# Kernel tuning notes

Hardware: AMD Instinct MI355X
Metric: run time of the kernel (lower is better)

Reference implementation:

```python
import jax, jax.numpy as jnp
import numpy as np


def setup_inputs() -> dict:
    key = jax.random.key(0)
    k1, k2 = jax.random.split(key)
    mesh_3D = jax.random.uniform(k1, (100, 100, 100, 3), dtype=jnp.float32)
    receiver_pos = jax.random.uniform(k2, (128, 3), dtype=jnp.float32)
    return {"mesh_3D": mesh_3D, "receiver_pos": receiver_pos}


def reference(mesh_3D, receiver_pos):
    # Flatten mesh to [L, 3]
    pts = mesh_3D.reshape(-1, 3)
    L = pts.shape[0]
    B = receiver_pos.shape[0]
    # Squared distances [B, L]; argmin of sqrt(d2) == argmin of d2 (sqrt is monotone),
    # so skipping the sqrt gives the same indices as the torch code.
    d2 = jnp.sum((receiver_pos[:, None, :] - pts[None, :, :]) ** 2, axis=-1)
    min_index = jnp.argmin(d2, axis=1).astype(jnp.int32)  # [B]
    # One-hot over the mesh. The original loop scatters with the *whole* min_index
    # tensor (zero-initialized) at every iteration, so for B > 1 index 0 also ends
    # up set to 1. We reproduce that behavior faithfully.
    one_hot = jnp.zeros((L, 1), dtype=pts.dtype).at[min_index, 0].set(1.0)
    if B > 1:
        one_hot = one_hot.at[0, 0].set(1.0)
    closest_points = pts[min_index]  # [B, 3]
    input_tensor = jnp.concatenate([pts, one_hot], axis=1).astype(jnp.float32)  # [L, 4]
    return input_tensor, closest_points, min_index
```

## Files before the change

### kernel.cpp

```cpp
#include <hip/hip_runtime.h>
#include <hip/hip_bf16.h>


#define NRECV 128
#define TILE 512
#define BLK 256
#define NGRP 4

typedef unsigned long long u64;

__global__ __launch_bounds__(BLK) void k_argmin_fill(
    const float* __restrict__ pts, const float* __restrict__ recv,
    u64* __restrict__ stage, float* __restrict__ out, int L, int ntiles) {
  __shared__ float4 sp4[TILE];
  __shared__ u64 sm[NGRP][NRECV];

  const int tid = threadIdx.x;
  const int g = tid >> 6;
  const int c = tid & 63;

  const float rx0 = recv[c * 3 + 0];
  const float ry0 = recv[c * 3 + 1];
  const float rz0 = recv[c * 3 + 2];
  const float rx1 = recv[(c + 64) * 3 + 0];
  const float ry1 = recv[(c + 64) * 3 + 1];
  const float rz1 = recv[(c + 64) * 3 + 2];

  float b0 = 3.4e38f, b1 = 3.4e38f;
  int i0 = 0, i1 = 0;

  for (int t = blockIdx.x; t < ntiles; t += gridDim.x) {
    const int base = t * TILE;
    const int cnt = min(TILE, L - base);

    for (int q = tid; q < cnt; q += BLK) {
      const int gi = base + q;
      float4 v;
      v.x = pts[3 * gi + 0];
      v.y = pts[3 * gi + 1];
      v.z = pts[3 * gi + 2];
      v.w = 0.0f;
      sp4[q] = v;
      reinterpret_cast<float4*>(out)[gi] = v;
    }
    __syncthreads();

#pragma unroll 4
    for (int p = g; p < cnt; p += NGRP) {
      const float4 q = sp4[p];
      const float dx0 = q.x - rx0, dy0 = q.y - ry0, dz0 = q.z - rz0;
      const float d0 = fmaf(dz0, dz0, fmaf(dy0, dy0, dx0 * dx0));
      const float dx1 = q.x - rx1, dy1 = q.y - ry1, dz1 = q.z - rz1;
      const float d1 = fmaf(dz1, dz1, fmaf(dy1, dy1, dx1 * dx1));
      const bool c0 = d0 < b0;
      b0 = c0 ? d0 : b0;
      i0 = c0 ? (base + p) : i0;
      const bool c1 = d1 < b1;
      b1 = c1 ? d1 : b1;
      i1 = c1 ? (base + p) : i1;
    }
    __syncthreads();
  }

  sm[g][c] = ((u64)__float_as_uint(b0) << 32) | (unsigned int)i0;
  sm[g][c + 64] = ((u64)__float_as_uint(b1) << 32) | (unsigned int)i1;
  __syncthreads();
  if (tid < NRECV) {
    u64 best = sm[0][tid];
#pragma unroll
    for (int k = 1; k < NGRP; ++k) {
      u64 o = sm[k][tid];
      best = o < best ? o : best;
    }
    stage[(size_t)blockIdx.x * NRECV + tid] = best;
  }
}

__global__ __launch_bounds__(BLK) void k_finalize(
    const u64* __restrict__ stage, int nblocks,
    const float* __restrict__ pts, float* __restrict__ out, int L) {
  const int r = blockIdx.x;
  const int tid = threadIdx.x;

  u64 best = ~0ull;
  for (int j = tid; j < nblocks; j += BLK) {
    u64 k = stage[(size_t)j * NRECV + r];
    best = k < best ? k : best;
  }
  for (int off = 32; off > 0; off >>= 1) {
    u64 o = __shfl_down(best, off);
    best = o < best ? o : best;
  }
  __shared__ u64 w[BLK / 64];
  if ((tid & 63) == 0) w[tid >> 6] = best;
  __syncthreads();
  if (tid == 0) {
#pragma unroll
    for (int i = 1; i < BLK / 64; ++i) {
      u64 o = w[i];
      best = o < best ? o : best;
    }
    const unsigned int idx = (unsigned int)(best & 0xffffffffu);
    const size_t Lo = (size_t)L * 4;
    out[Lo + (size_t)r * 3 + 0] = pts[(size_t)idx * 3 + 0];
    out[Lo + (size_t)r * 3 + 1] = pts[(size_t)idx * 3 + 1];
    out[Lo + (size_t)r * 3 + 2] = pts[(size_t)idx * 3 + 2];
    out[Lo + (size_t)NRECV * 3 + r] = (float)idx;
    out[(size_t)idx * 4 + 3] = 1.0f;
    if (r == 0) out[3] = 1.0f;
  }
}

extern "C" void kernel_launch(void* const* d_in, const int* in_sizes, int n_in,
                              void* d_out, int out_size, void* d_ws, size_t ws_size,
                              hipStream_t stream) {
  const float* pts = (const float*)d_in[0];
  const float* recv = (const float*)d_in[1];
  float* out = (float*)d_out;

  const int L = in_sizes[0] / 3;
  const int ntiles = (L + TILE - 1) / TILE;

  int nb1 = 1024;
  if ((size_t)nb1 * NRECV * sizeof(u64) > ws_size) {
    nb1 = (int)(ws_size / (NRECV * sizeof(u64)));
    if (nb1 < 1) nb1 = 1;
  }
  if (nb1 > ntiles) nb1 = ntiles;

  u64* stage = (u64*)d_ws;

  k_argmin_fill<<<nb1, BLK, 0, stream>>>(pts, recv, stage, out, L, ntiles);
  k_finalize<<<NRECV, BLK, 0, stream>>>(stage, nb1, pts, out, L);
}
```

Before: 96.82 us.

## Use 4 receivers per thread and atomicMin banks for cross-block argmin

The main kernel now uses 512-thread blocks. Each thread handles 4 receivers (32-lane halves of each wave take alternating points), and the two half-wave results are merged with a shuffle. Instead of writing per-block partials to a large staging buffer scanned by a 128-block finalize, blocks atomicMin packed (distance,index) keys into 4 padded banks of cells. A tiny single-block finalize then reads those cells, at the cost of an extra init kernel launch and atomic contention. A sentinel point is also written past the end of a partial tile so the paired-lane loop does not read garbage.

```diff
diff --git a/kernel.cpp b/kernel.cpp
--- a/kernel.cpp
+++ b/kernel.cpp
@@ -1,114 +1,119 @@
 #include <hip/hip_runtime.h>
-#include <hip/hip_bf16.h>
 
 
 #define NRECV 128
 #define TILE 512
-#define BLK 256
-#define NGRP 4
+#define BLK 512
+#define NWAVE (BLK / 64)
+#define CELL_STRIDE 16
 
 typedef unsigned long long u64;
 
-__global__ __launch_bounds__(BLK) void k_argmin_fill(
+__global__ __launch_bounds__(128) void k_init(u64* __restrict__ cells, int n) {
+  int i = blockIdx.x * 128 + threadIdx.x;
+  if (i < n) cells[i] = ~0ull;
+}
+
+__global__ __launch_bounds__(BLK) void k_main(
     const float* __restrict__ pts, const float* __restrict__ recv,
-    u64* __restrict__ stage, float* __restrict__ out, int L, int ntiles) {
-  __shared__ float4 sp4[TILE];
-  __shared__ u64 sm[NGRP][NRECV];
+    u64* __restrict__ cells, int nbanks, float* __restrict__ out,
+    int L, int ntiles) {
+  __shared__ float4 sp4[TILE + 1];
+  __shared__ u64 sm[NWAVE][NRECV];
 
   const int tid = threadIdx.x;
   const int g = tid >> 6;
-  const int c = tid & 63;
+  const int c = tid & 31;
+  const int ph = (tid >> 5) & 1;
 
-  const float rx0 = recv[c * 3 + 0];
-  const float ry0 = recv[c * 3 + 1];
-  const float rz0 = recv[c * 3 + 2];
-  const float rx1 = recv[(c + 64) * 3 + 0];
-  const float ry1 = recv[(c + 64) * 3 + 1];
-  const float rz1 = recv[(c + 64) * 3 + 2];
+  float rx[4], ry[4], rz[4];
+#pragma unroll
+  for (int k = 0; k < 4; ++k) {
+    rx[k] = recv[(c + 32 * k) * 3 + 0];
+    ry[k] = recv[(c + 32 * k) * 3 + 1];
+    rz[k] = recv[(c + 32 * k) * 3 + 2];
+  }
 
-  float b0 = 3.4e38f, b1 = 3.4e38f;
-  int i0 = 0, i1 = 0;
+  float bd[4] = {1e30f, 1e30f, 1e30f, 1e30f};
+  int bi[4] = {0, 0, 0, 0};
 
   for (int t = blockIdx.x; t < ntiles; t += gridDim.x) {
     const int base = t * TILE;
     const int cnt = min(TILE, L - base);
 
-    for (int q = tid; q < cnt; q += BLK) {
-      const int gi = base + q;
+    if (tid < cnt) {
+      const int gi = base + tid;
       float4 v;
       v.x = pts[3 * gi + 0];
       v.y = pts[3 * gi + 1];
       v.z = pts[3 * gi + 2];
       v.w = 0.0f;
-      sp4[q] = v;
+      sp4[tid] = v;
       reinterpret_cast<float4*>(out)[gi] = v;
     }
+    if (tid == 0 && cnt < TILE)
+      sp4[cnt] = make_float4(1e30f, 1e30f, 1e30f, 0.0f);
     __syncthreads();
 
-#pragma unroll 4
-    for (int p = g; p < cnt; p += NGRP) {
+#pragma unroll 2
+    for (int p2 = 2 * g; p2 < cnt; p2 += 2 * NWAVE) {
+      const int p = p2 + ph;
       const float4 q = sp4[p];
-      const float dx0 = q.x - rx0, dy0 = q.y - ry0, dz0 = q.z - rz0;
-      const float d0 = fmaf(dz0, dz0, fmaf(dy0, dy0, dx0 * dx0));
-      const float dx1 = q.x - rx1, dy1 = q.y - ry1, dz1 = q.z - rz1;
-      const float d1 = fmaf(dz1, dz1, fmaf(dy1, dy1, dx1 * dx1));
-      const bool c0 = d0 < b0;
-      b0 = c0 ? d0 : b0;
-      i0 = c0 ? (base + p) : i0;
-      const bool c1 = d1 < b1;
-      b1 = c1 ? d1 : b1;
-      i1 = c1 ? (base + p) : i1;
+#pragma unroll
+      for (int k = 0; k < 4; ++k) {
+        const float dx = q.x - rx[k];
+        const float dy = q.y - ry[k];
+        const float dz = q.z - rz[k];
+        const float d = fmaf(dz, dz, fmaf(dy, dy, dx * dx));
+        const bool cc = d < bd[k];
+        bd[k] = cc ? d : bd[k];
+        bi[k] = cc ? (base + p) : bi[k];
+      }
     }
     __syncthreads();
   }
 
-  sm[g][c] = ((u64)__float_as_uint(b0) << 32) | (unsigned int)i0;
-  sm[g][c + 64] = ((u64)__float_as_uint(b1) << 32) | (unsigned int)i1;
+  u64 key[4];
+#pragma unroll
+  for (int k = 0; k < 4; ++k) {
+    key[k] = ((u64)__float_as_uint(bd[k]) << 32) | (unsigned int)bi[k];
+    const u64 o = __shfl_xor(key[k], 32, 64);
+    key[k] = o < key[k] ? o : key[k];
+  }
+  if (ph == 0) {
+#pragma unroll
+    for (int k = 0; k < 4; ++k) sm[g][c + 32 * k] = key[k];
+  }
   __syncthreads();
   if (tid < NRECV) {
     u64 best = sm[0][tid];
 #pragma unroll
-    for (int k = 1; k < NGRP; ++k) {
-      u64 o = sm[k][tid];
+    for (int w = 1; w < NWAVE; ++w) {
+      const u64 o = sm[w][tid];
       best = o < best ? o : best;
     }
-    stage[(size_t)blockIdx.x * NRECV + tid] = best;
+    const int bank = blockIdx.x & (nbanks - 1);
+    atomicMin(&cells[(size_t)(bank * NRECV + tid) * CELL_STRIDE], best);
   }
 }
 
-__global__ __launch_bounds__(BLK) void k_finalize(
-    const u64* __restrict__ stage, int nblocks,
+__global__ __launch_bounds__(128) void k_finalize(
+    const u64* __restrict__ cells, int nbanks,
     const float* __restrict__ pts, float* __restrict__ out, int L) {
-  const int r = blockIdx.x;
-  const int tid = threadIdx.x;
-
+  const int r = threadIdx.x;
   u64 best = ~0ull;
-  for (int j = tid; j < nblocks; j += BLK) {
-    u64 k = stage[(size_t)j * NRECV + r];
-    best = k < best ? k : best;
-  }
-  for (int off = 32; off > 0; off >>= 1) {
-    u64 o = __shfl_down(best, off);
+  for (int b = 0; b < nbanks; ++b) {
+    const u64 o = cells[(size_t)(b * NRECV + r) * CELL_STRIDE];
     best = o < best ? o : best;
   }
-  __shared__ u64 w[BLK / 64];
-  if ((tid & 63) == 0) w[tid >> 6] = best;
-  __syncthreads();
-  if (tid == 0) {
-#pragma unroll
-    for (int i = 1; i < BLK / 64; ++i) {
-      u64 o = w[i];
-      best = o < best ? o : best;
-    }
-    const unsigned int idx = (unsigned int)(best & 0xffffffffu);
-    const size_t Lo = (size_t)L * 4;
-    out[Lo + (size_t)r * 3 + 0] = pts[(size_t)idx * 3 + 0];
-    out[Lo + (size_t)r * 3 + 1] = pts[(size_t)idx * 3 + 1];
-    out[Lo + (size_t)r * 3 + 2] = pts[(size_t)idx * 3 + 2];
-    out[Lo + (size_t)NRECV * 3 + r] = (float)idx;
-    out[(size_t)idx * 4 + 3] = 1.0f;
-    if (r == 0) out[3] = 1.0f;
-  }
+  const unsigned int idx = (unsigned int)(best & 0xffffffffu);
+  const size_t Lo = (size_t)L * 4;
+  out[Lo + (size_t)r * 3 + 0] = pts[(size_t)idx * 3 + 0];
+  out[Lo + (size_t)r * 3 + 1] = pts[(size_t)idx * 3 + 1];
+  out[Lo + (size_t)r * 3 + 2] = pts[(size_t)idx * 3 + 2];
+  out[Lo + (size_t)NRECV * 3 + r] = (float)idx;
+  out[(size_t)idx * 4 + 3] = 1.0f;
+  if (r == 0) out[3] = 1.0f;
 }
 
 extern "C" void kernel_launch(void* const* d_in, const int* in_sizes, int n_in,
@@ -117,19 +122,19 @@
   const float* pts = (const float*)d_in[0];
   const float* recv = (const float*)d_in[1];
   float* out = (float*)d_out;
+  u64* cells = (u64*)d_ws;
 
   const int L = in_sizes[0] / 3;
   const int ntiles = (L + TILE - 1) / TILE;
 
-  int nb1 = 1024;
-  if ((size_t)nb1 * NRECV * sizeof(u64) > ws_size) {
-    nb1 = (int)(ws_size / (NRECV * sizeof(u64)));
-    if (nb1 < 1) nb1 = 1;
-  }
-  if (nb1 > ntiles) nb1 = ntiles;
+  const int nbanks =
+      (ws_size >= (size_t)4 * NRECV * CELL_STRIDE * sizeof(u64)) ? 4 : 1;
+  const int ncell_u64 = nbanks * NRECV * CELL_STRIDE;
 
-  u64* stage = (u64*)d_ws;
+  int grid = 512;
+  if (grid > ntiles) grid = ntiles;
 
-  k_argmin_fill<<<nb1, BLK, 0, stream>>>(pts, recv, stage, out, L, ntiles);
-  k_finalize<<<NRECV, BLK, 0, stream>>>(stage, nb1, pts, out, L);
+  k_init<<<(ncell_u64 + 127) / 128, 128, 0, stream>>>(cells, ncell_u64);
+  k_main<<<grid, BLK, 0, stream>>>(pts, recv, cells, nbanks, out, L, ntiles);
+  k_finalize<<<1, 128, 0, stream>>>(cells, nbanks, pts, out, L);
 }
```

After: 98.35 us. About the same (+1.6%).
